# Optimization experiments

Measured on AMD Instinct MI355X. Metric: run time of the kernel, lower is better.

## Reference

```python
import jax, jax.numpy as jnp
import numpy as np

EMBED_DIM = 1024
NUM_HEADS = 16
DIM_HEAD = EMBED_DIM // NUM_HEADS


def setup_inputs() -> dict:
    key = jax.random.key(0)
    ks = jax.random.split(key, 9)
    s = 1.0 / np.sqrt(EMBED_DIM)
    x = jax.random.normal(ks[0], (2, 2048, EMBED_DIM), dtype=jnp.float32)
    Wq = jax.random.uniform(ks[1], (EMBED_DIM, EMBED_DIM), jnp.float32, -s, s)
    bq = jax.random.uniform(ks[2], (EMBED_DIM,), jnp.float32, -s, s)
    Wk = jax.random.uniform(ks[3], (EMBED_DIM, EMBED_DIM), jnp.float32, -s, s)
    bk = jax.random.uniform(ks[4], (EMBED_DIM,), jnp.float32, -s, s)
    Wv = jax.random.uniform(ks[5], (EMBED_DIM, EMBED_DIM), jnp.float32, -s, s)
    bv = jax.random.uniform(ks[6], (EMBED_DIM,), jnp.float32, -s, s)
    Wo = jax.random.uniform(ks[7], (EMBED_DIM, EMBED_DIM), jnp.float32, -s, s)
    bo = jax.random.uniform(ks[8], (EMBED_DIM,), jnp.float32, -s, s)
    return {"x": x, "Wq": Wq, "bq": bq, "Wk": Wk, "bk": bk,
            "Wv": Wv, "bv": bv, "Wo": Wo, "bo": bo}


def reference(x, Wq, bq, Wk, bk, Wv, bv, Wo, bo):
    B, S, _ = x.shape
    # Linear layers (torch nn.Linear: x @ W.T + b), reshape to heads
    Q = (x @ Wq.T + bq).reshape(B, S, NUM_HEADS, DIM_HEAD)
    K = (x @ Wk.T + bk).reshape(B, S, NUM_HEADS, DIM_HEAD)
    V = (x @ Wv.T + bv).reshape(B, S, NUM_HEADS, DIM_HEAD)
    scores = jnp.einsum('bqhd,bkhd->bhqk', Q, K) / np.sqrt(DIM_HEAD)
    attn = jax.nn.softmax(scores, axis=-1)
    context = jnp.einsum('bhqk,bkhd->bqhd', attn, V).reshape(B, S, EMBED_DIM)
    return context @ Wo.T + bo
```

## Files before the change

kernel.cpp:

```cpp
#include <hip/hip_runtime.h>
#include <hip/hip_bf16.h>

#define SEQ   2048
#define EMB   1024
#define NHEAD 16
#define DHEAD 64
#define BATCH 2
#define MTOT  (BATCH*SEQ)
#define QT    128
#define KT    64
#define NTILE (SEQ/KT)

typedef __attribute__((ext_vector_type(8))) short s8v;
typedef __attribute__((ext_vector_type(4))) short s4v;
typedef __attribute__((ext_vector_type(4))) float f4v;

__device__ __forceinline__ short f2b(float f) {
    union { float fl; unsigned u; } v; v.fl = f;
    unsigned u = v.u;
    u = (u + 0x7fffu + ((u >> 16) & 1u)) >> 16;
    return (short)u;
}
__device__ __forceinline__ unsigned pk2(float a, float b) {
    union { __hip_bfloat162 h; unsigned u; } c;
    c.h = __float22bfloat162_rn(float2{a, b});
    return c.u;
}

#if __has_builtin(__builtin_amdgcn_exp2f)
__device__ __forceinline__ float exp2_fast(float x) { return __builtin_amdgcn_exp2f(x); }
#else
__device__ __forceinline__ float exp2_fast(float x) { return exp2f(x); }
#endif

__device__ __forceinline__ void pl32swap(unsigned &a, unsigned &b) {
    asm("v_permlane32_swap_b32 %0, %1" : "+v"(a), "+v"(b));
}
__device__ __forceinline__ void pl16swap(unsigned &a, unsigned &b) {
    asm("v_permlane16_swap_b32 %0, %1" : "+v"(a), "+v"(b));
}

__device__ __forceinline__ void bar_lds() {
    asm volatile("s_waitcnt lgkmcnt(0)\n\ts_barrier" ::: "memory");
}

__device__ __forceinline__ void gl_lds16(const short* g, short* l) {
    __builtin_amdgcn_global_load_lds(
        (const __attribute__((address_space(1))) void*)g,
        (__attribute__((address_space(3))) void*)l, 16, 0, 0);
}

__global__ __launch_bounds__(256)
void cvt_swz(const float* __restrict__ s0, const float* __restrict__ s1,
             const float* __restrict__ s2, const float* __restrict__ s3,
             const float* __restrict__ s4,
             short* __restrict__ d0, short* __restrict__ d1,
             short* __restrict__ d2, short* __restrict__ d3,
             short* __restrict__ d4)
{
    const int seg = blockIdx.y;
    const float* s = seg == 0 ? s0 : seg == 1 ? s1 : seg == 2 ? s2 : seg == 3 ? s3 : s4;
    short*       d = seg == 0 ? d0 : seg == 1 ? d1 : seg == 2 ? d2 : seg == 3 ? d3 : d4;
    const int nchunk = (seg == 0 ? MTOT * EMB : EMB * EMB) / 8;
    const int stride = gridDim.x * 256;
    for (int i = blockIdx.x * 256 + threadIdx.x; i < nchunk; i += stride) {
        const int row = i >> 7;
        const int c   = i & 127;
        const float4 v0 = *(const float4*)(s + (size_t)i * 8);
        const float4 v1 = *(const float4*)(s + (size_t)i * 8 + 4);
        s8v o;
        o[0] = f2b(v0.x); o[1] = f2b(v0.y); o[2] = f2b(v0.z); o[3] = f2b(v0.w);
        o[4] = f2b(v1.x); o[5] = f2b(v1.y); o[6] = f2b(v1.z); o[7] = f2b(v1.w);
        const int cp = (c & ~7) | ((c & 7) ^ (row & 7));
        *(s8v*)(d + (size_t)row * EMB + cp * 8) = o;
    }
}

template<int NT, bool FUSED3>
__global__ __launch_bounds__(256, 3)
void gemm_bb3(const short* __restrict__ A,
              const short* __restrict__ W0, const short* __restrict__ W1, const short* __restrict__ W2,
              const float* __restrict__ B0, const float* __restrict__ B1, const float* __restrict__ B2,
              void* __restrict__ C0, void* __restrict__ C1, void* __restrict__ C2)
{
    constexpr int JN = NT / 32;
    const int K = EMB, N = EMB;
    const int ntiles = EMB / NT;
    const int mat = blockIdx.x / ntiles;
    const int n0  = (blockIdx.x % ntiles) * NT;
    const int m0  = blockIdx.y * 128;
    const short* W  = (mat == 0) ? W0 : (mat == 1 ? W1 : W2);
    const float* Bi = (mat == 0) ? B0 : (mat == 1 ? B1 : B2);
    void*        C  = (mat == 0) ? C0 : (mat == 1 ? C1 : C2);
    const float qscale = (FUSED3 && mat == 0) ? 0.18033688f : 1.0f;

    __shared__ __align__(16) short As[128 * 64];
    __shared__ __align__(16) short Ws[NT * 64];

    const int tid  = threadIdx.x;
    const int lane = tid & 63;
    const int wave = tid >> 6;
    const int quad = lane >> 4;
    const int l16  = lane & 15;
    const int l8   = l16 & 7;
    const int wm   = wave >> 1;
    const int wn   = wave & 1;

    f4v acc[4][JN] = {};

    const int srow = lane >> 3;
    const int scol = (lane & 7) * 8;

    for (int k0 = 0; k0 < K; k0 += 64) {
        #pragma unroll
        for (int p = 0; p < 4; ++p) {
            const int rbase = wave * 32 + p * 8;
            gl_lds16(A + (size_t)(m0 + rbase + srow) * K + k0 + scol,
                     As + rbase * 64);
        }
        #pragma unroll
        for (int p = 0; p < NT / 32; ++p) {
            const int rbase = wave * (NT / 4) + p * 8;
            gl_lds16(W + (size_t)(n0 + rbase + srow) * K + k0 + scol,
                     Ws + rbase * 64);
        }
        __syncthreads();

        #pragma unroll
        for (int kk = 0; kk < 2; ++kk) {
            const int slot = ((kk * 4 + quad) ^ l8) * 8;
            s8v af[4], wf[JN];
            #pragma unroll
            for (int i = 0; i < 4; ++i)
                af[i] = *(const s8v*)(As + (wm * 64 + i * 16 + l16) * 64 + slot);
            #pragma unroll
            for (int j = 0; j < JN; ++j)
                wf[j] = *(const s8v*)(Ws + (wn * (NT / 2) + j * 16 + l16) * 64 + slot);
            #pragma unroll
            for (int i = 0; i < 4; ++i)
                #pragma unroll
                for (int j = 0; j < JN; ++j)
                    acc[i][j] = __builtin_amdgcn_mfma_f32_16x16x32_bf16(
                        af[i], wf[j], acc[i][j], 0, 0, 0);
        }
        __syncthreads();
    }

    #pragma unroll
    for (int j = 0; j < JN; ++j) {
        const int n = n0 + wn * (NT / 2) + j * 16 + l16;
        const float bv = Bi[n];
        #pragma unroll
        for (int i = 0; i < 4; ++i) {
            const int mb = m0 + wm * 64 + i * 16 + quad * 4;
            if (FUSED3 && mat == 2) {
                const int bb = mb >> 11, s = mb & 2047;
                s4v ov;
                #pragma unroll
                for (int rr = 0; rr < 4; ++rr) ov[rr] = f2b(acc[i][j][rr] + bv);
                *(s4v*)((short*)C + ((size_t)(bb * 1024 + n)) * SEQ + s) = ov;
            } else if (FUSED3) {
                #pragma unroll
                for (int rr = 0; rr < 4; ++rr)
                    ((short*)C)[(size_t)(mb + rr) * N + n] = f2b((acc[i][j][rr] + bv) * qscale);
            } else {
                #pragma unroll
                for (int rr = 0; rr < 4; ++rr)
                    ((float*)C)[(size_t)(mb + rr) * N + n] = acc[i][j][rr] + bv;
            }
        }
    }
}

__global__ __launch_bounds__(512, 4)
void attn_mfma7(const short* Q, const short* __restrict__ Kg,
                const short* __restrict__ Vt, short* O)
{
    const int i    = blockIdx.x;
    const int xcd  = i & 7;
    const int slot = i >> 3;
    const int combo = xcd * 4 + (slot >> 4);
    const int qb = slot & 15;
    const int h  = combo & 15;
    const int b  = combo >> 4;
    const int q0 = qb * QT;

    const int tid  = threadIdx.x;
    const int lane = tid & 63;
    const int wave = tid >> 6;
    const int quad = lane >> 4;
    const int l16  = lane & 15;
    const int l8   = l16 & 7;

    __shared__ __align__(16) short Ks[2][64 * 64];
    __shared__ __align__(16) short Vs[2][64 * 64];

    s8v qf[2];
    #pragma unroll
    for (int kk = 0; kk < 2; ++kk)
        qf[kk] = *(const s8v*)(Q + (size_t)(b * SEQ + q0 + wave * 16 + l16) * EMB
                                 + h * DHEAD + kk * 32 + quad * 8);

    f4v oacc[4] = {};
    f4v sacc    = {};
    s8v onef;
    #pragma unroll
    for (int e = 0; e < 8; ++e) onef[e] = (short)0x3F80;

    const int r = lane >> 3, c = lane & 7;
    const int sc8 = (c ^ r) * 8;
    const bool isK = wave < 4;
    const int wrow = (wave & 3) * 16;
    const size_t kbase = (size_t)(b * SEQ) * EMB + h * DHEAD;
    const size_t vbase = (size_t)((b * NHEAD + h) * DHEAD) * SEQ;
    const short* gsrc = isK ? Kg + kbase + (size_t)(wrow + r) * EMB + sc8
                            : Vt + vbase + (size_t)(wrow + r) * SEQ + sc8;
    const size_t gstep8 = isK ? (size_t)8 * EMB : (size_t)8 * SEQ;
    const size_t tstep  = isK ? (size_t)KT * EMB : (size_t)KT;
    short* const lbase  = (isK ? (short*)Ks : (short*)Vs) + wrow * 64;

    gl_lds16(gsrc,          lbase);
    gl_lds16(gsrc + gstep8, lbase + 8 * 64);
    const short* gnext = gsrc + tstep;

    for (int t = 0; t < NTILE; ++t) {
        const int buf = t & 1;
        __syncthreads();
        if (t + 1 < NTILE) {
            short* ldst = lbase + (buf ^ 1) * (64 * 64);
            gl_lds16(gnext,          ldst);
            gl_lds16(gnext + gstep8, ldst + 8 * 64);
            gnext += tstep;
        }
        const short* KsB = Ks[buf];
        const short* VsB = Vs[buf];

        f4v sc[4] = {};
        #pragma unroll
        for (int kk = 0; kk < 2; ++kk) {
            const int ko = ((kk * 4 + quad) ^ l8) * 8;
            s8v kf[4];
            #pragma unroll
            for (int j = 0; j < 4; ++j)
                kf[j] = *(const s8v*)(KsB + (j * 16 + l16) * 64 + ko);
            #pragma unroll
            for (int j = 0; j < 4; ++j)
                sc[j] = __builtin_amdgcn_mfma_f32_16x16x32_bf16(
                    kf[j], qf[kk], sc[j], 0, 0, 0);
        }

        unsigned u[4][2];
        #pragma unroll
        for (int j = 0; j < 4; ++j) {
            u[j][0] = pk2(exp2_fast(sc[j][0]), exp2_fast(sc[j][1]));
            u[j][1] = pk2(exp2_fast(sc[j][2]), exp2_fast(sc[j][3]));
        }

        #pragma unroll
        for (int r2 = 0; r2 < 2; ++r2) {
            pl32swap(u[0][r2], u[1][r2]);
            pl32swap(u[2][r2], u[3][r2]);
            pl16swap(u[0][r2], u[1][r2]);
            pl16swap(u[2][r2], u[3][r2]);
        }
        union { unsigned uu[4]; s8v s; } pfa, pfb;
        pfa.uu[0] = u[0][0]; pfa.uu[1] = u[0][1]; pfa.uu[2] = u[1][0]; pfa.uu[3] = u[1][1];
        pfb.uu[0] = u[2][0]; pfb.uu[1] = u[2][1]; pfb.uu[2] = u[3][0]; pfb.uu[3] = u[3][1];

        #pragma unroll
        for (int kk = 0; kk < 2; ++kk) {
            const s8v pf = kk ? pfb.s : pfa.s;
            sacc = __builtin_amdgcn_mfma_f32_16x16x32_bf16(onef, pf, sacc, 0, 0, 0);
            const int ko = ((kk * 4 + quad) ^ l8) * 8;
            #pragma unroll
            for (int j = 0; j < 4; ++j) {
                const s8v vf = *(const s8v*)(VsB + (j * 16 + l16) * 64 + ko);
                oacc[j] = __builtin_amdgcn_mfma_f32_16x16x32_bf16(
                    vf, pf, oacc[j], 0, 0, 0);
            }
        }
    }

    const float inv = 1.0f / sacc[0];

    __syncthreads();
    short* Os = (short*)Ks;
    #pragma unroll
    for (int j = 0; j < 4; ++j) {
        union { unsigned uu[2]; s4v s; } ov;
        ov.uu[0] = pk2(oacc[j][0] * inv, oacc[j][1] * inv);
        ov.uu[1] = pk2(oacc[j][2] * inv, oacc[j][3] * inv);
        const int pc = ((j * 2 + (quad >> 1)) ^ l8) * 8 + (quad & 1) * 4;
        *(s4v*)(Os + (wave * 16 + l16) * 64 + pc) = ov.s;
    }
    bar_lds();

    const int row = tid >> 2;
    const int cb  = (tid & 3) * 2;
    #pragma unroll
    for (int c4 = 0; c4 < 2; ++c4) {
        const int pcc = cb + c4;
        const s8v tt = *(const s8v*)(Os + row * 64 + pcc * 8);
        *(s8v*)(O + (size_t)(b * SEQ + q0 + row) * EMB + h * DHEAD + pcc * 8) = tt;
    }
}

extern "C" void kernel_launch(void* const* d_in, const int* in_sizes, int n_in,
                              void* d_out, int out_size, void* d_ws, size_t ws_size,
                              hipStream_t stream)
{
    const float* x  = (const float*)d_in[0];
    const float* Wq = (const float*)d_in[1];
    const float* bq = (const float*)d_in[2];
    const float* Wk = (const float*)d_in[3];
    const float* bk = (const float*)d_in[4];
    const float* Wv = (const float*)d_in[5];
    const float* bv = (const float*)d_in[6];
    const float* Wo = (const float*)d_in[7];
    const float* bo = (const float*)d_in[8];
    float* out = (float*)d_out;

    short* xb  = (short*)d_ws;
    short* Wqb = xb  + (size_t)MTOT * EMB;
    short* Wkb = Wqb + (size_t)EMB * EMB;
    short* Wvb = Wkb + (size_t)EMB * EMB;
    short* Wob = Wvb + (size_t)EMB * EMB;
    short* Qw  = Wob + (size_t)EMB * EMB;
    short* Kw  = Qw  + (size_t)MTOT * EMB;
    short* Vtw = Kw  + (size_t)MTOT * EMB;

    cvt_swz<<<dim3(512, 5), 256, 0, stream>>>(x, Wq, Wk, Wv, Wo,
                                              xb, Wqb, Wkb, Wvb, Wob);

    gemm_bb3<128, true><<<dim3(24, 32), 256, 0, stream>>>(
        xb, Wqb, Wkb, Wvb, bq, bk, bv, Qw, Kw, Vtw);

    attn_mfma7<<<dim3(BATCH * NHEAD * (SEQ / QT)), 512, 0, stream>>>(Qw, Kw, Vtw, Qw);

    gemm_bb3<64, false><<<dim3(16, 32), 256, 0, stream>>>(
        Qw, Wob, Wob, Wob, bo, bo, bo, out, out, out);
}
```

Baseline: 185.3 us.

## Software-pipeline attention loop so PV of previous tile overlaps QK of current

Result: no change. 182.3 us (-1.6%).

```diff
diff --git a/kernel.cpp b/kernel.cpp
--- a/kernel.cpp
+++ b/kernel.cpp
@@ -173,7 +173,7 @@
 }
 
 __global__ __launch_bounds__(512, 4)
-void attn_mfma7(const short* Q, const short* __restrict__ Kg,
+void attn_mfma8(const short* Q, const short* __restrict__ Kg,
                 const short* __restrict__ Vt, short* O)
 {
     const int i    = blockIdx.x;
@@ -193,7 +193,7 @@
     const int l8   = l16 & 7;
 
     __shared__ __align__(16) short Ks[2][64 * 64];
-    __shared__ __align__(16) short Vs[2][64 * 64];
+    __shared__ __align__(16) short Vs[3][64 * 64];
 
     s8v qf[2];
     #pragma unroll
@@ -217,69 +217,105 @@
                             : Vt + vbase + (size_t)(wrow + r) * SEQ + sc8;
     const size_t gstep8 = isK ? (size_t)8 * EMB : (size_t)8 * SEQ;
     const size_t tstep  = isK ? (size_t)KT * EMB : (size_t)KT;
-    short* const lbase  = (isK ? (short*)Ks : (short*)Vs) + wrow * 64;
-
-    gl_lds16(gsrc,          lbase);
-    gl_lds16(gsrc + gstep8, lbase + 8 * 64);
+    short* const lbK = (short*)Ks + wrow * 64;
+    short* const lbV = (short*)Vs + wrow * 64;
+
+    {
+        short* l0 = isK ? lbK : lbV;
+        gl_lds16(gsrc,          l0);
+        gl_lds16(gsrc + gstep8, l0 + 8 * 64);
+    }
     const short* gnext = gsrc + tstep;
 
-    for (int t = 0; t < NTILE; ++t) {
-        const int buf = t & 1;
+    s8v pfA_prev, pfB_prev;
+
+#define QK_BLOCK(KSB)                                                        \
+    f4v scv[4] = {};                                                         \
+    _Pragma("unroll")                                                        \
+    for (int kk = 0; kk < 2; ++kk) {                                         \
+        const int ko = ((kk * 4 + quad) ^ l8) * 8;                           \
+        s8v kf[4];                                                           \
+        _Pragma("unroll")                                                    \
+        for (int j = 0; j < 4; ++j)                                          \
+            kf[j] = *(const s8v*)((KSB) + (j * 16 + l16) * 64 + ko);         \
+        _Pragma("unroll")                                                    \
+        for (int j = 0; j < 4; ++j)                                          \
+            scv[j] = __builtin_amdgcn_mfma_f32_16x16x32_bf16(                \
+                kf[j], qf[kk], scv[j], 0, 0, 0);                             \
+    }
+
+#define SM_BLOCK()                                                           \
+    unsigned u[4][2];                                                        \
+    _Pragma("unroll")                                                        \
+    for (int j = 0; j < 4; ++j) {                                            \
+        u[j][0] = pk2(exp2_fast(scv[j][0]), exp2_fast(scv[j][1]));           \
+        u[j][1] = pk2(exp2_fast(scv[j][2]), exp2_fast(scv[j][3]));           \
+    }                                                                        \
+    _Pragma("unroll")                                                        \
+    for (int r2 = 0; r2 < 2; ++r2) {                                         \
+        pl32swap(u[0][r2], u[1][r2]);                                        \
+        pl32swap(u[2][r2], u[3][r2]);                                        \
+        pl16swap(u[0][r2], u[1][r2]);                                        \
+        pl16swap(u[2][r2], u[3][r2]);                                        \
+    }                                                                        \
+    union { unsigned uu[4]; s8v s; } pfa, pfb;                               \
+    pfa.uu[0] = u[0][0]; pfa.uu[1] = u[0][1];                                \
+    pfa.uu[2] = u[1][0]; pfa.uu[3] = u[1][1];                                \
+    pfb.uu[0] = u[2][0]; pfb.uu[1] = u[2][1];                                \
+    pfb.uu[2] = u[3][0]; pfb.uu[3] = u[3][1];
+
+#define PV_BLOCK(VSB)                                                        \
+    _Pragma("unroll")                                                        \
+    for (int kk = 0; kk < 2; ++kk) {                                         \
+        const s8v pf = kk ? pfB_prev : pfA_prev;                             \
+        sacc = __builtin_amdgcn_mfma_f32_16x16x32_bf16(onef, pf, sacc, 0, 0, 0); \
+        const int ko = ((kk * 4 + quad) ^ l8) * 8;                           \
+        _Pragma("unroll")                                                    \
+        for (int j = 0; j < 4; ++j) {                                        \
+            const s8v vf = *(const s8v*)((VSB) + (j * 16 + l16) * 64 + ko);  \
+            oacc[j] = __builtin_amdgcn_mfma_f32_16x16x32_bf16(               \
+                vf, pf, oacc[j], 0, 0, 0);                                   \
+        }                                                                    \
+    }
+
+    {
         __syncthreads();
-        if (t + 1 < NTILE) {
-            short* ldst = lbase + (buf ^ 1) * (64 * 64);
+        short* ldst = (isK ? lbK : lbV) + 64 * 64;
+        gl_lds16(gnext,          ldst);
+        gl_lds16(gnext + gstep8, ldst + 8 * 64);
+        gnext += tstep;
+
+        QK_BLOCK((const short*)Ks)
+        SM_BLOCK()
+        pfA_prev = pfa.s; pfB_prev = pfb.s;
+    }
+
+    for (int t = 1; t < NTILE; ++t) {
+        __syncthreads();
+        const int tp1 = t + 1;
+        if (tp1 < NTILE) {
+            short* ldst = isK ? lbK + (tp1 & 1) * (64 * 64)
+                              : lbV + (tp1 % 3) * (64 * 64);
             gl_lds16(gnext,          ldst);
             gl_lds16(gnext + gstep8, ldst + 8 * 64);
             gnext += tstep;
         }
-        const short* KsB = Ks[buf];
-        const short* VsB = Vs[buf];
-
-        f4v sc[4] = {};
-        #pragma unroll
-        for (int kk = 0; kk < 2; ++kk) {
-            const int ko = ((kk * 4 + quad) ^ l8) * 8;
-            s8v kf[4];
-            #pragma unroll
-            for (int j = 0; j < 4; ++j)
-                kf[j] = *(const s8v*)(KsB + (j * 16 + l16) * 64 + ko);
-            #pragma unroll
-            for (int j = 0; j < 4; ++j)
-                sc[j] = __builtin_amdgcn_mfma_f32_16x16x32_bf16(
-                    kf[j], qf[kk], sc[j], 0, 0, 0);
-        }
-
-        unsigned u[4][2];
-        #pragma unroll
-        for (int j = 0; j < 4; ++j) {
-            u[j][0] = pk2(exp2_fast(sc[j][0]), exp2_fast(sc[j][1]));
-            u[j][1] = pk2(exp2_fast(sc[j][2]), exp2_fast(sc[j][3]));
-        }
-
-        #pragma unroll
-        for (int r2 = 0; r2 < 2; ++r2) {
-            pl32swap(u[0][r2], u[1][r2]);
-            pl32swap(u[2][r2], u[3][r2]);
-            pl16swap(u[0][r2], u[1][r2]);
-            pl16swap(u[2][r2], u[3][r2]);
-        }
-        union { unsigned uu[4]; s8v s; } pfa, pfb;
-        pfa.uu[0] = u[0][0]; pfa.uu[1] = u[0][1]; pfa.uu[2] = u[1][0]; pfa.uu[3] = u[1][1];
-        pfb.uu[0] = u[2][0]; pfb.uu[1] = u[2][1]; pfb.uu[2] = u[3][0]; pfb.uu[3] = u[3][1];
-
-        #pragma unroll
-        for (int kk = 0; kk < 2; ++kk) {
-            const s8v pf = kk ? pfb.s : pfa.s;
-            sacc = __builtin_amdgcn_mfma_f32_16x16x32_bf16(onef, pf, sacc, 0, 0, 0);
-            const int ko = ((kk * 4 + quad) ^ l8) * 8;
-            #pragma unroll
-            for (int j = 0; j < 4; ++j) {
-                const s8v vf = *(const s8v*)(VsB + (j * 16 + l16) * 64 + ko);
-                oacc[j] = __builtin_amdgcn_mfma_f32_16x16x32_bf16(
-                    vf, pf, oacc[j], 0, 0, 0);
-            }
-        }
-    }
+        const short* KsB = (const short*)Ks + (t & 1) * (64 * 64);
+        const short* VsB = (const short*)Vs + ((t - 1) % 3) * (64 * 64);
+
+        QK_BLOCK(KsB)
+        SM_BLOCK()
+        PV_BLOCK(VsB)
+        pfA_prev = pfa.s; pfB_prev = pfb.s;
+    }
+
+    {
+        const short* VsB = (const short*)Vs + ((NTILE - 1) % 3) * (64 * 64);
+        PV_BLOCK(VsB)
+    }
+#undef QK_BLOCK
+#undef SM_BLOCK
+#undef PV_BLOCK
 
     const float inv = 1.0f / sacc[0];
 
@@ -335,7 +371,7 @@
     gemm_bb3<128, true><<<dim3(24, 32), 256, 0, stream>>>(
         xb, Wqb, Wkb, Wvb, bq, bk, bv, Qw, Kw, Vtw);
 
-    attn_mfma7<<<dim3(BATCH * NHEAD * (SEQ / QT)), 512, 0, stream>>>(Qw, Kw, Vtw, Qw);
+    attn_mfma8<<<dim3(BATCH * NHEAD * (SEQ / QT)), 512, 0, stream>>>(Qw, Kw, Vtw, Qw);
 
     gemm_bb3<64, false><<<dim3(16, 32), 256, 0, stream>>>(
         Qw, Wob, Wob, Wob, bo, bo, bo, out, out, out);
```
